# Kernel tuning notes

Hardware: AMD Instinct MI355X
Metric: run time of the kernel (lower is better)

The kernel has to match this reference:

```python
import jax, jax.numpy as jnp
import numpy as np
import math

C, H, W = 3, 4096, 4096
B = 8            # block_size
K = 16           # keep_coeffs
COEFF_SCALE = 1.0
NH, NW = H // B, W // B
N = C * NH * NW * K  # total_params = 12_582_912


def _zigzag_indices(b):
    idx = []
    for s in range(2 * b - 1):
        if s % 2 == 0:
            for i in range(s + 1):
                j = s - i
                if i < b and j < b:
                    idx.append((i, j))
        else:
            for j in range(s + 1):
                i = s - j
                if i < b and j < b:
                    idx.append((i, j))
    return idx


def _flat_indices():
    # ptr ordering in torch sample(): c outer, then bh, bw, then zig-zag coeff
    zz = np.asarray(_zigzag_indices(B)[:K], dtype=np.int64)  # (K, 2)
    c = np.arange(C)[:, None, None, None]
    bh = np.arange(NH)[None, :, None, None]
    bw = np.arange(NW)[None, None, :, None]
    u = zz[:, 0][None, None, None, :]
    v = zz[:, 1][None, None, None, :]
    flat = c * (H * W) + (bh * B + u) * W + (bw * B + v)  # (C, NH, NW, K)
    return flat.reshape(-1).astype(np.int32)


def setup_inputs() -> dict:
    key = jax.random.key(0)
    k1, k2 = jax.random.split(key)
    mean = jax.random.normal(k1, (N,), dtype=jnp.float32)
    log_std = jnp.full((N,), -4.0, dtype=jnp.float32)
    eps = jax.random.normal(k2, (N,), dtype=jnp.float32)
    flat_idx = jnp.asarray(_flat_indices())
    return {"mean": mean, "log_std": log_std, "eps": eps, "flat_idx": flat_idx}


def reference(mean, log_std, eps, flat_idx):
    std = jnp.exp(log_std)
    sample = (mean + std * eps) * COEFF_SCALE  # (N,)
    # single vectorized scatter (indices are disjoint by construction)
    coeffs = jnp.zeros((C * H * W,), dtype=jnp.float32).at[flat_idx].set(
        sample, unique_indices=True).reshape(C, H, W)
    log2pi = math.log(2.0 * math.pi)
    log_prob = -0.5 * jnp.sum(eps * eps + 2.0 * log_std + log2pi)
    entropy = jnp.sum(0.5 * (1.0 + log2pi) + log_std)
    return coeffs, log_prob, entropy
```

## Files before the change

### kernel.cpp

```cpp
#include <hip/hip_runtime.h>


constexpr int W = 4096;
constexpr int H = 4096;
constexpr long long CHW = 3LL * 4096 * 4096;
constexpr float LOG2PI = 1.8378770664093453f;
constexpr int NBLK = 12288;
constexpr float NTOT = 12582912.0f;

__device__ __constant__ unsigned long long RT[8] = {
    0xFFFFFF0A09030200ull,
    0xFFFFFFFF0B080401ull,
    0xFFFFFFFFFF0C0705ull,
    0xFFFFFFFFFFFF0D06ull,
    0xFFFFFFFFFFFFFF0Eull,
    0xFFFFFFFFFFFFFF0Full,
    0xFFFFFFFFFFFFFFFFull,
    0xFFFFFFFFFFFFFFFFull
};

__global__ __launch_bounds__(256) void dct_policy_kernel(
    const float* __restrict__ mean,
    const float* __restrict__ log_std,
    const float* __restrict__ eps,
    float* __restrict__ out,
    float2* __restrict__ partials)
{
    __shared__ float smp[64 * 17];
    __shared__ float p1[4], p2[4];

    const int t   = threadIdx.x;
    const int bid = blockIdx.x;
    const int c   = bid >> 12;
    const int rem = bid & 4095;
    const int bh  = rem >> 3;
    const int sx  = rem & 7;

    const long long pbase = (long long)(c * 512 + bh) * 8192 + (long long)sx * 1024;

    const float4 m4 = *(const float4*)(mean    + pbase + 4 * t);
    const float4 l4 = *(const float4*)(log_std + pbase + 4 * t);
    const float4 e4 = *(const float4*)(eps     + pbase + 4 * t);

    const float mv[4] = {m4.x, m4.y, m4.z, m4.w};
    const float lv[4] = {l4.x, l4.y, l4.z, l4.w};
    const float ev[4] = {e4.x, e4.y, e4.z, e4.w};

    float s1 = 0.f, s2 = 0.f;
#pragma unroll
    for (int j = 0; j < 4; ++j) {
        const int idx  = 4 * t + j;
        const int tile = idx >> 4;
        const int rank = idx & 15;
        const float s  = mv[j] + __builtin_expf(lv[j]) * ev[j];
        smp[tile * 17 + rank] = s;
        s1 += ev[j] * ev[j];
        s2 += lv[j];
    }

#pragma unroll
    for (int off = 32; off > 0; off >>= 1) {
        s1 += __shfl_xor(s1, off, 64);
        s2 += __shfl_xor(s2, off, 64);
    }
    if ((t & 63) == 0) { p1[t >> 6] = s1; p2[t >> 6] = s2; }

    __syncthreads();

    if (t == 0) {
        partials[bid] = make_float2(p1[0] + p1[1] + p1[2] + p1[3],
                                    p2[0] + p2[1] + p2[2] + p2[3]);
    }

    const long long obase = (long long)c * ((long long)H * W)
                          + (long long)(bh * 8) * W + sx * 512;
#pragma unroll
    for (int q = 0; q < 4; ++q) {
        const int f    = t + 256 * q;
        const int u    = f >> 7;
        const int x4   = f & 127;
        const int tile = x4 >> 1;
        const int vb   = (x4 & 1) * 4;
        const unsigned long long row = RT[u];
        float4 o;
        float* ov = (float*)&o;
#pragma unroll
        for (int j = 0; j < 4; ++j) {
            const unsigned r = (unsigned)((row >> (8 * (vb + j))) & 0xFFull);
            const float v = smp[tile * 17 + (int)(r & 15u)];
            ov[j] = (r != 0xFFu) ? v : 0.0f;
        }
        *(float4*)(out + obase + (long long)u * W + x4 * 4) = o;
    }
}

__global__ __launch_bounds__(256) void reduce_kernel(
    const float2* __restrict__ partials,
    float* __restrict__ out)
{
    const int t = threadIdx.x;
    float s1 = 0.f, s2 = 0.f;
    for (int i = t; i < NBLK; i += 256) {
        const float2 v = partials[i];
        s1 += v.x;
        s2 += v.y;
    }
#pragma unroll
    for (int off = 32; off > 0; off >>= 1) {
        s1 += __shfl_xor(s1, off, 64);
        s2 += __shfl_xor(s2, off, 64);
    }
    __shared__ float a1[4], a2[4];
    if ((t & 63) == 0) { a1[t >> 6] = s1; a2[t >> 6] = s2; }
    __syncthreads();
    if (t == 0) {
        const float S1 = a1[0] + a1[1] + a1[2] + a1[3];
        const float S2 = a2[0] + a2[1] + a2[2] + a2[3];
        out[CHW]     = -0.5f * S1 - S2 - 0.5f * NTOT * LOG2PI;
        out[CHW + 1] = 0.5f * (1.0f + LOG2PI) * NTOT + S2;
    }
}

extern "C" void kernel_launch(void* const* d_in, const int* in_sizes, int n_in,
                              void* d_out, int out_size, void* d_ws, size_t ws_size,
                              hipStream_t stream) {
    const float* mean    = (const float*)d_in[0];
    const float* log_std = (const float*)d_in[1];
    const float* eps     = (const float*)d_in[2];
    float* out = (float*)d_out;
    float2* partials = (float2*)d_ws;

    dct_policy_kernel<<<NBLK, 256, 0, stream>>>(mean, log_std, eps, out, partials);
    reduce_kernel<<<1, 256, 0, stream>>>(partials, out);
}
```

Measured before the change: 339.9 us.

## Split fused kernel into producer and scatter-writer kernels with nontemporal stores

Splits the single fused kernel into two. A producer computes the samples and per-block partial sums and writes them to a workspace buffer. A writer then reads the samples and scatters them into the zero-padded output, using nontemporal stores to keep the large output stream out of cache. This adds an extra 50 MB round trip through global memory plus a kernel launch, betting that simpler kernels and nontemporal writes make up for it.

```diff
diff --git a/kernel.cpp b/kernel.cpp
--- a/kernel.cpp
+++ b/kernel.cpp
@@ -4,9 +4,12 @@
 constexpr int W = 4096;
 constexpr int H = 4096;
 constexpr long long CHW = 3LL * 4096 * 4096;
+constexpr long long NPAR = 12582912;
 constexpr float LOG2PI = 1.8378770664093453f;
 constexpr int NBLK = 12288;
 constexpr float NTOT = 12582912.0f;
+
+typedef float f32x4 __attribute__((ext_vector_type(4)));
 
 __device__ __constant__ unsigned long long RT[8] = {
     0xFFFFFF0A09030200ull,
@@ -19,15 +22,48 @@
     0xFFFFFFFFFFFFFFFFull
 };
 
-__global__ __launch_bounds__(256) void dct_policy_kernel(
+__global__ __launch_bounds__(256) void producer_kernel(
     const float* __restrict__ mean,
     const float* __restrict__ log_std,
     const float* __restrict__ eps,
-    float* __restrict__ out,
+    float* __restrict__ smp_out,
     float2* __restrict__ partials)
 {
+    const int t = threadIdx.x;
+    const long long g = (long long)blockIdx.x * 1024 + 4 * t;
+
+    const float4 m4 = *(const float4*)(mean    + g);
+    const float4 l4 = *(const float4*)(log_std + g);
+    const float4 e4 = *(const float4*)(eps     + g);
+
+    float4 s4;
+    s4.x = m4.x + __builtin_expf(l4.x) * e4.x;
+    s4.y = m4.y + __builtin_expf(l4.y) * e4.y;
+    s4.z = m4.z + __builtin_expf(l4.z) * e4.z;
+    s4.w = m4.w + __builtin_expf(l4.w) * e4.w;
+    *(float4*)(smp_out + g) = s4;
+
+    float s1 = e4.x * e4.x + e4.y * e4.y + e4.z * e4.z + e4.w * e4.w;
+    float s2 = l4.x + l4.y + l4.z + l4.w;
+#pragma unroll
+    for (int off = 32; off > 0; off >>= 1) {
+        s1 += __shfl_xor(s1, off, 64);
+        s2 += __shfl_xor(s2, off, 64);
+    }
+    __shared__ float p1[4], p2[4];
+    if ((t & 63) == 0) { p1[t >> 6] = s1; p2[t >> 6] = s2; }
+    __syncthreads();
+    if (t == 0) {
+        partials[blockIdx.x] = make_float2(p1[0] + p1[1] + p1[2] + p1[3],
+                                           p2[0] + p2[1] + p2[2] + p2[3]);
+    }
+}
+
+__global__ __launch_bounds__(256) void writer_kernel(
+    const float* __restrict__ smp_in,
+    float* __restrict__ out)
+{
     __shared__ float smp[64 * 17];
-    __shared__ float p1[4], p2[4];
 
     const int t   = threadIdx.x;
     const int bid = blockIdx.x;
@@ -37,40 +73,14 @@
     const int sx  = rem & 7;
 
     const long long pbase = (long long)(c * 512 + bh) * 8192 + (long long)sx * 1024;
-
-    const float4 m4 = *(const float4*)(mean    + pbase + 4 * t);
-    const float4 l4 = *(const float4*)(log_std + pbase + 4 * t);
-    const float4 e4 = *(const float4*)(eps     + pbase + 4 * t);
-
-    const float mv[4] = {m4.x, m4.y, m4.z, m4.w};
-    const float lv[4] = {l4.x, l4.y, l4.z, l4.w};
-    const float ev[4] = {e4.x, e4.y, e4.z, e4.w};
-
-    float s1 = 0.f, s2 = 0.f;
+    const float4 s4 = *(const float4*)(smp_in + pbase + 4 * t);
+    const float sv[4] = {s4.x, s4.y, s4.z, s4.w};
 #pragma unroll
     for (int j = 0; j < 4; ++j) {
-        const int idx  = 4 * t + j;
-        const int tile = idx >> 4;
-        const int rank = idx & 15;
-        const float s  = mv[j] + __builtin_expf(lv[j]) * ev[j];
-        smp[tile * 17 + rank] = s;
-        s1 += ev[j] * ev[j];
-        s2 += lv[j];
+        const int idx = 4 * t + j;
+        smp[(idx >> 4) * 17 + (idx & 15)] = sv[j];
     }
-
-#pragma unroll
-    for (int off = 32; off > 0; off >>= 1) {
-        s1 += __shfl_xor(s1, off, 64);
-        s2 += __shfl_xor(s2, off, 64);
-    }
-    if ((t & 63) == 0) { p1[t >> 6] = s1; p2[t >> 6] = s2; }
-
     __syncthreads();
-
-    if (t == 0) {
-        partials[bid] = make_float2(p1[0] + p1[1] + p1[2] + p1[3],
-                                    p2[0] + p2[1] + p2[2] + p2[3]);
-    }
 
     const long long obase = (long long)c * ((long long)H * W)
                           + (long long)(bh * 8) * W + sx * 512;
@@ -82,15 +92,15 @@
         const int tile = x4 >> 1;
         const int vb   = (x4 & 1) * 4;
         const unsigned long long row = RT[u];
-        float4 o;
-        float* ov = (float*)&o;
+        f32x4 o;
 #pragma unroll
         for (int j = 0; j < 4; ++j) {
             const unsigned r = (unsigned)((row >> (8 * (vb + j))) & 0xFFull);
             const float v = smp[tile * 17 + (int)(r & 15u)];
-            ov[j] = (r != 0xFFu) ? v : 0.0f;
+            o[j] = (r != 0xFFu) ? v : 0.0f;
         }
-        *(float4*)(out + obase + (long long)u * W + x4 * 4) = o;
+        __builtin_nontemporal_store(
+            o, (f32x4*)(out + obase + (long long)u * W + x4 * 4));
     }
 }
 
@@ -128,8 +138,11 @@
     const float* log_std = (const float*)d_in[1];
     const float* eps     = (const float*)d_in[2];
     float* out = (float*)d_out;
-    float2* partials = (float2*)d_ws;
 
-    dct_policy_kernel<<<NBLK, 256, 0, stream>>>(mean, log_std, eps, out, partials);
+    float*  samples  = (float*)d_ws;
+    float2* partials = (float2*)((char*)d_ws + NPAR * 4);
+
+    producer_kernel<<<NBLK, 256, 0, stream>>>(mean, log_std, eps, samples, partials);
+    writer_kernel<<<NBLK, 256, 0, stream>>>(samples, out);
     reduce_kernel<<<1, 256, 0, stream>>>(partials, out);
 }
```

After: 350.3 us. +3.1%, slower.
